# Optimization experiments

Measured on AMD Instinct MI355X. Metric: run time of the kernel, lower is better.

The kernel has to match this reference:

```python
import jax, jax.numpy as jnp
import numpy as np

B, DIM, D_IN, HID, N_HID_EXTRA = 65536, 128, 64, 512, 2  # num_hidden_layers=3 -> 2 extra hidden linears
LOG_SCALE_CLAMP = 2.0


def _mlp(x, Win, bin_, Whid, bhid, Wout, bout):
    # torch nn.Linear: y = x @ W.T + b
    h = jax.nn.relu(x @ Win.T + bin_)
    for i in range(Whid.shape[0]):  # fixed small layer loop
        h = jax.nn.relu(h @ Whid[i].T + bhid[i])
    return h @ Wout.T + bout


def setup_inputs() -> dict:
    key = jax.random.key(0)
    ks = jax.random.split(key, 13)
    w = lambda k, shp: (jax.random.normal(k, shp, dtype=jnp.float32) * 0.05)
    d_out = DIM - D_IN
    return {
        "z": jax.random.normal(ks[0], (B, DIM), dtype=jnp.float32),
        "s_Win": w(ks[1], (HID, D_IN)),   "s_bin": jnp.zeros((HID,), jnp.float32),
        "s_Whid": w(ks[2], (N_HID_EXTRA, HID, HID)), "s_bhid": jnp.zeros((N_HID_EXTRA, HID), jnp.float32),
        "s_Wout": w(ks[3], (d_out, HID)), "s_bout": jnp.zeros((d_out,), jnp.float32),
        "t_Win": w(ks[4], (HID, D_IN)),   "t_bin": jnp.zeros((HID,), jnp.float32),
        "t_Whid": w(ks[5], (N_HID_EXTRA, HID, HID)), "t_bhid": jnp.zeros((N_HID_EXTRA, HID), jnp.float32),
        "t_Wout": w(ks[6], (d_out, HID)), "t_bout": jnp.zeros((d_out,), jnp.float32),
    }


def reference(z, s_Win, s_bin, s_Whid, s_bhid, s_Wout, s_bout,
              t_Win, t_bin, t_Whid, t_bhid, t_Wout, t_bout):
    # mask = first D_IN dims -> gather reduces to slicing
    z1 = z[:, :D_IN]   # (B, d_in)  passthrough half
    z2 = z[:, D_IN:]   # (B, d_out) transformed half
    log_s = jnp.clip(_mlp(z1, s_Win, s_bin, s_Whid, s_bhid, s_Wout, s_bout),
                     -LOG_SCALE_CLAMP, LOG_SCALE_CLAMP)
    t = _mlp(z1, t_Win, t_bin, t_Whid, t_bhid, t_Wout, t_bout)
    z2_out = z2 * jnp.exp(log_s) + t
    z_out = jnp.concatenate([z1, z2_out], axis=1)  # scatter back per mask
    log_det = log_s.sum(axis=-1)                   # (B,)
    return (z_out, log_det)
```

## Files before the change

### kernel.cpp

```cpp
#include <hip/hip_runtime.h>
#include <stdint.h>


#define NROWS 65536
#define RPB   128
#define NBLK  (NROWS / RPB)

#define OFF_S_WIN   0
#define OFF_S_WHID  32768
#define OFF_S_WOUT  557056
#define OFF_T_WIN   589824
#define OFF_T_WHID  622592
#define OFF_T_WOUT  1146880
#define W_ELEMS     1179648

typedef __attribute__((ext_vector_type(8))) short short8;
typedef __attribute__((ext_vector_type(4))) float f32x4;

__device__ __forceinline__ uint32_t f2bf1(float f) {
  uint32_t u = __float_as_uint(f);
  return (u + 0x7fffu + ((u >> 16) & 1u)) >> 16;
}
__device__ __forceinline__ uint32_t pk2bf(float a, float b) {
  return f2bf1(a) | (f2bf1(b) << 16);
}

__global__ void cvt_weights(const float* __restrict__ sWin, const float* __restrict__ sWhid,
                            const float* __restrict__ sWout, const float* __restrict__ tWin,
                            const float* __restrict__ tWhid, const float* __restrict__ tWout,
                            uint16_t* __restrict__ wbf) {
  int g = blockIdx.x * blockDim.x + threadIdx.x;
  int e = g * 4;
  if (e >= W_ELEMS) return;
  const float* src; int off;
  if      (e < OFF_S_WHID) { src = sWin;  off = e; }
  else if (e < OFF_S_WOUT) { src = sWhid; off = e - OFF_S_WHID; }
  else if (e < OFF_T_WIN)  { src = sWout; off = e - OFF_S_WOUT; }
  else if (e < OFF_T_WHID) { src = tWin;  off = e - OFF_T_WIN; }
  else if (e < OFF_T_WOUT) { src = tWhid; off = e - OFF_T_WHID; }
  else                     { src = tWout; off = e - OFF_T_WOUT; }
  f32x4 v = *(const f32x4*)(src + off);
  uint2 r; r.x = pk2bf(v.x, v.y); r.y = pk2bf(v.z, v.w);
  *(uint2*)(wbf + e) = r;
}

template<bool BF>
__device__ __forceinline__ short8 ldW(const uint16_t* __restrict__ wb,
                                      const float* __restrict__ wf, int idx) {
  if (BF) {
    return *(const short8*)(wb + idx);
  } else {
    f32x4 x = *(const f32x4*)(wf + idx);
    f32x4 y = *(const f32x4*)(wf + idx + 4);
    short8 r;
    r[0] = (short)f2bf1(x.x); r[1] = (short)f2bf1(x.y);
    r[2] = (short)f2bf1(x.z); r[3] = (short)f2bf1(x.w);
    r[4] = (short)f2bf1(y.x); r[5] = (short)f2bf1(y.y);
    r[6] = (short)f2bf1(y.z); r[7] = (short)f2bf1(y.w);
    return r;
  }
}

__device__ __forceinline__ short8 ldsB(const uint16_t* buf, int row, int k) {
  int byte = (row * 1024 + k * 2) ^ ((row & 7) << 4);
  return *(const short8*)((const char*)buf + byte);
}

__device__ __forceinline__ void store_h(f32x4 acc[4][8], const float* __restrict__ bias,
                                        uint16_t* hdst, int wave, int lane) {
  const int l15 = lane & 15, lq = lane >> 4;
  __syncthreads();
  #pragma unroll
  for (int rt = 0; rt < 4; ++rt) {
    const int n0 = wave * 64 + rt * 16 + lq * 4;
    f32x4 bv = *(const f32x4*)(bias + n0);
    #pragma unroll
    for (int ct = 0; ct < 8; ++ct) {
      const int row = ct * 16 + l15;
      f32x4 v = acc[rt][ct] + bv;
      uint2 p;
      p.x = pk2bf(fmaxf(v.x, 0.f), fmaxf(v.y, 0.f));
      p.y = pk2bf(fmaxf(v.z, 0.f), fmaxf(v.w, 0.f));
      int byte = (row * 1024 + n0 * 2) ^ ((row & 7) << 4);
      *(uint2*)((char*)hdst + byte) = p;
    }
  }
  __syncthreads();
}

template<bool BF>
__device__ __forceinline__ void dense_in(
    const uint16_t* __restrict__ wb, const float* __restrict__ wf,
    const float* __restrict__ bias, const float* __restrict__ z, long rowbase,
    uint16_t* hdst, int wave, int lane) {
  const int l15 = lane & 15, lq = lane >> 4;
  f32x4 acc[4][8];
  #pragma unroll
  for (int rt = 0; rt < 4; ++rt)
    #pragma unroll
    for (int ct = 0; ct < 8; ++ct) acc[rt][ct] = (f32x4){0.f, 0.f, 0.f, 0.f};
  const int wbase = (wave * 64 + l15) * 64 + lq * 8;
  #pragma unroll
  for (int k0 = 0; k0 < 64; k0 += 32) {
    short8 a[4];
    #pragma unroll
    for (int rt = 0; rt < 4; ++rt) a[rt] = ldW<BF>(wb, wf, wbase + rt * 1024 + k0);
    #pragma unroll
    for (int ct = 0; ct < 8; ++ct) {
      const float* zp = z + (rowbase + ct * 16 + l15) * 128 + lq * 8 + k0;
      f32x4 u = *(const f32x4*)zp;
      f32x4 v = *(const f32x4*)(zp + 4);
      short8 b;
      b[0] = (short)f2bf1(u.x); b[1] = (short)f2bf1(u.y);
      b[2] = (short)f2bf1(u.z); b[3] = (short)f2bf1(u.w);
      b[4] = (short)f2bf1(v.x); b[5] = (short)f2bf1(v.y);
      b[6] = (short)f2bf1(v.z); b[7] = (short)f2bf1(v.w);
      #pragma unroll
      for (int rt = 0; rt < 4; ++rt)
        acc[rt][ct] = __builtin_amdgcn_mfma_f32_16x16x32_bf16(a[rt], b, acc[rt][ct], 0, 0, 0);
    }
  }
  store_h(acc, bias, hdst, wave, lane);
}

template<bool BF>
__device__ __forceinline__ void dense_relu512(
    const uint16_t* __restrict__ wb, const float* __restrict__ wf,
    const float* __restrict__ bias, uint16_t* hbuf, int wave, int lane) {
  const int l15 = lane & 15, lq = lane >> 4;
  f32x4 acc[4][8];
  #pragma unroll
  for (int rt = 0; rt < 4; ++rt)
    #pragma unroll
    for (int ct = 0; ct < 8; ++ct) acc[rt][ct] = (f32x4){0.f, 0.f, 0.f, 0.f};
  const int wbase = (wave * 64 + l15) * 512 + lq * 8;

  short8 an[4];
  #pragma unroll
  for (int rt = 0; rt < 4; ++rt) an[rt] = ldW<BF>(wb, wf, wbase + rt * 8192);

  #pragma unroll 2
  for (int k0 = 0; k0 < 512; k0 += 32) {
    short8 ac[4];
    #pragma unroll
    for (int rt = 0; rt < 4; ++rt) ac[rt] = an[rt];
    if (k0 + 32 < 512) {
      #pragma unroll
      for (int rt = 0; rt < 4; ++rt)
        an[rt] = ldW<BF>(wb, wf, wbase + rt * 8192 + k0 + 32);
    }
    #pragma unroll
    for (int ct = 0; ct < 8; ++ct) {
      short8 b = ldsB(hbuf, ct * 16 + l15, lq * 8 + k0);
      #pragma unroll
      for (int rt = 0; rt < 4; ++rt)
        acc[rt][ct] = __builtin_amdgcn_mfma_f32_16x16x32_bf16(ac[rt], b, acc[rt][ct], 0, 0, 0);
    }
  }
  store_h(acc, bias, hbuf, wave, lane);
}

template<bool BF>
__device__ __forceinline__ void final_layer(
    const uint16_t* __restrict__ wb, const float* __restrict__ wf,
    const uint16_t* hbuf, int wave, int lane, f32x4 acc[4][2]) {
  const int l15 = lane & 15, lq = lane >> 4;
  #pragma unroll
  for (int rt = 0; rt < 4; ++rt)
    #pragma unroll
    for (int ct = 0; ct < 2; ++ct) acc[rt][ct] = (f32x4){0.f, 0.f, 0.f, 0.f};
  const int wbase = l15 * 512 + lq * 8;
  #pragma unroll 4
  for (int k0 = 0; k0 < 512; k0 += 32) {
    short8 a[4];
    #pragma unroll
    for (int rt = 0; rt < 4; ++rt) a[rt] = ldW<BF>(wb, wf, wbase + rt * 8192 + k0);
    #pragma unroll
    for (int ct = 0; ct < 2; ++ct) {
      short8 b = ldsB(hbuf, wave * 32 + ct * 16 + l15, lq * 8 + k0);
      #pragma unroll
      for (int rt = 0; rt < 4; ++rt)
        acc[rt][ct] = __builtin_amdgcn_mfma_f32_16x16x32_bf16(a[rt], b, acc[rt][ct], 0, 0, 0);
    }
  }
}

template<bool BF>
__global__ __launch_bounds__(512, 2) void coupling(
    const float* __restrict__ z,
    const float* __restrict__ sWin, const float* __restrict__ sbin,
    const float* __restrict__ sWhid, const float* __restrict__ sbhid,
    const float* __restrict__ sWout, const float* __restrict__ sbout,
    const float* __restrict__ tWin, const float* __restrict__ tbin,
    const float* __restrict__ tWhid, const float* __restrict__ tbhid,
    const float* __restrict__ tWout, const float* __restrict__ tbout,
    const uint16_t* __restrict__ wbf, float* __restrict__ out) {
  extern __shared__ __align__(16) uint16_t h[];
  const int tid = threadIdx.x;
  const int wave = tid >> 6, lane = tid & 63;
  const int l15 = lane & 15, lq = lane >> 4;
  const long rowbase = (long)blockIdx.x * RPB;

  dense_in<BF>(wbf + OFF_S_WIN, sWin, sbin, z, rowbase, h, wave, lane);
  dense_relu512<BF>(wbf + OFF_S_WHID, sWhid, sbhid, h, wave, lane);
  dense_relu512<BF>(wbf + OFF_S_WHID + 262144, sWhid + 262144, sbhid + 512, h, wave, lane);

  if (wave < 4) {
    f32x4 acc[4][2];
    final_layer<BF>(wbf + OFF_S_WOUT, sWout, h, wave, lane, acc);
    #pragma unroll
    for (int ct = 0; ct < 2; ++ct) {
      const long row = rowbase + wave * 32 + ct * 16 + l15;
      float sum = 0.f;
      #pragma unroll
      for (int rt = 0; rt < 4; ++rt) {
        f32x4 bv = *(const f32x4*)(sbout + rt * 16 + lq * 4);
        f32x4 v = acc[rt][ct] + bv;
        v.x = fminf(fmaxf(v.x, -2.f), 2.f);
        v.y = fminf(fmaxf(v.y, -2.f), 2.f);
        v.z = fminf(fmaxf(v.z, -2.f), 2.f);
        v.w = fminf(fmaxf(v.w, -2.f), 2.f);
        sum += v.x + v.y + v.z + v.w;
        *(f32x4*)(out + row * 128 + 64 + rt * 16 + lq * 4) = v;
      }
      sum += __shfl_xor(sum, 16, 64);
      sum += __shfl_xor(sum, 32, 64);
      if (lane < 16) out[(long)NROWS * 128 + row] = sum;
    }
  } else {
    #pragma unroll
    for (int i = 0; i < 8; ++i) {
      int v = (wave - 4) * 64 + lane + i * 256;
      int row = v >> 4, kc = (v & 15) * 4;
      *(f32x4*)(out + (rowbase + row) * 128 + kc) =
          *(const f32x4*)(z + (rowbase + row) * 128 + kc);
    }
  }
  __syncthreads();

  dense_in<BF>(wbf + OFF_T_WIN, tWin, tbin, z, rowbase, h, wave, lane);
  dense_relu512<BF>(wbf + OFF_T_WHID, tWhid, tbhid, h, wave, lane);
  dense_relu512<BF>(wbf + OFF_T_WHID + 262144, tWhid + 262144, tbhid + 512, h, wave, lane);

  if (wave < 4) {
    f32x4 acc[4][2];
    final_layer<BF>(wbf + OFF_T_WOUT, tWout, h, wave, lane, acc);
    #pragma unroll
    for (int ct = 0; ct < 2; ++ct) {
      const long row = rowbase + wave * 32 + ct * 16 + l15;
      #pragma unroll
      for (int rt = 0; rt < 4; ++rt) {
        f32x4 bv = *(const f32x4*)(tbout + rt * 16 + lq * 4);
        f32x4 tv = acc[rt][ct] + bv;
        const long o = row * 128 + 64 + rt * 16 + lq * 4;
        f32x4 ls = *(const f32x4*)(out + o);
        f32x4 z2 = *(const f32x4*)(z + o);
        f32x4 r;
        r.x = z2.x * __expf(ls.x) + tv.x;
        r.y = z2.y * __expf(ls.y) + tv.y;
        r.z = z2.z * __expf(ls.z) + tv.z;
        r.w = z2.w * __expf(ls.w) + tv.w;
        *(f32x4*)(out + o) = r;
      }
    }
  }
}

extern "C" void kernel_launch(void* const* d_in, const int* in_sizes, int n_in,
                              void* d_out, int out_size, void* d_ws, size_t ws_size,
                              hipStream_t stream) {
  const float* z     = (const float*)d_in[0];
  const float* sWin  = (const float*)d_in[1];
  const float* sbin  = (const float*)d_in[2];
  const float* sWhid = (const float*)d_in[3];
  const float* sbhid = (const float*)d_in[4];
  const float* sWout = (const float*)d_in[5];
  const float* sbout = (const float*)d_in[6];
  const float* tWin  = (const float*)d_in[7];
  const float* tbin  = (const float*)d_in[8];
  const float* tWhid = (const float*)d_in[9];
  const float* tbhid = (const float*)d_in[10];
  const float* tWout = (const float*)d_in[11];
  const float* tbout = (const float*)d_in[12];
  float* out = (float*)d_out;
  const size_t lds_bytes = (size_t)RPB * 512 * sizeof(uint16_t);

  if (ws_size >= (size_t)W_ELEMS * sizeof(uint16_t)) {
    uint16_t* wbf = (uint16_t*)d_ws;
    cvt_weights<<<W_ELEMS / 4 / 256, 256, 0, stream>>>(sWin, sWhid, sWout, tWin, tWhid, tWout, wbf);
    coupling<true><<<NBLK, 512, lds_bytes, stream>>>(z, sWin, sbin, sWhid, sbhid, sWout, sbout,
                                                     tWin, tbin, tWhid, tbhid, tWout, tbout, wbf, out);
  } else {
    coupling<false><<<NBLK, 512, lds_bytes, stream>>>(z, sWin, sbin, sWhid, sbhid, sWout, sbout,
                                                      tWin, tbin, tWhid, tbhid, tWout, tbout,
                                                      (const uint16_t*)d_in[1], out);
  }
}
```

Before: 234.8 us.

## Pad LDS row stride and double-buffer operands in hidden-layer MFMA loop

Replaces the XOR-swizzled LDS layout for the hidden activations with a padded row stride of 1040 bytes, so accesses avoid bank conflicts without the swizzle arithmetic. The 512x512 hidden-layer loop becomes an explicitly double-buffered pipeline: both weight and LDS activation fragments for the next k-slice are prefetched into registers while the current slice's MFMAs run. s_setprio raises wave priority around the MFMA bursts. The cost is more registers held per wave, and the LDS allocation grows slightly.

```diff
diff --git a/kernel.cpp b/kernel.cpp
--- a/kernel.cpp
+++ b/kernel.cpp
@@ -5,6 +5,7 @@
 #define NROWS 65536
 #define RPB   128
 #define NBLK  (NROWS / RPB)
+#define HSTR  1040
 
 #define OFF_S_WIN   0
 #define OFF_S_WHID  32768
@@ -62,8 +63,7 @@
 }
 
 __device__ __forceinline__ short8 ldsB(const uint16_t* buf, int row, int k) {
-  int byte = (row * 1024 + k * 2) ^ ((row & 7) << 4);
-  return *(const short8*)((const char*)buf + byte);
+  return *(const short8*)((const char*)buf + row * HSTR + k * 2);
 }
 
 __device__ __forceinline__ void store_h(f32x4 acc[4][8], const float* __restrict__ bias,
@@ -81,8 +81,7 @@
       uint2 p;
       p.x = pk2bf(fmaxf(v.x, 0.f), fmaxf(v.y, 0.f));
       p.y = pk2bf(fmaxf(v.z, 0.f), fmaxf(v.w, 0.f));
-      int byte = (row * 1024 + n0 * 2) ^ ((row & 7) << 4);
-      *(uint2*)((char*)hdst + byte) = p;
+      *(uint2*)((char*)hdst + row * HSTR + n0 * 2) = p;
     }
   }
   __syncthreads();
@@ -134,28 +133,42 @@
     #pragma unroll
     for (int ct = 0; ct < 8; ++ct) acc[rt][ct] = (f32x4){0.f, 0.f, 0.f, 0.f};
   const int wbase = (wave * 64 + l15) * 512 + lq * 8;
-
-  short8 an[4];
-  #pragma unroll
-  for (int rt = 0; rt < 4; ++rt) an[rt] = ldW<BF>(wb, wf, wbase + rt * 8192);
-
-  #pragma unroll 2
-  for (int k0 = 0; k0 < 512; k0 += 32) {
-    short8 ac[4];
-    #pragma unroll
-    for (int rt = 0; rt < 4; ++rt) ac[rt] = an[rt];
-    if (k0 + 32 < 512) {
+  const char* bbase = (const char*)hbuf + l15 * HSTR + lq * 16;
+
+  short8 a0[4], a1[4], b0[8], b1[8];
+  #pragma unroll
+  for (int rt = 0; rt < 4; ++rt) a0[rt] = ldW<BF>(wb, wf, wbase + rt * 8192);
+  #pragma unroll
+  for (int ct = 0; ct < 8; ++ct) b0[ct] = *(const short8*)(bbase + ct * 16 * HSTR);
+
+  #pragma unroll 1
+  for (int k0 = 0; k0 < 512; k0 += 64) {
+    #pragma unroll
+    for (int rt = 0; rt < 4; ++rt) a1[rt] = ldW<BF>(wb, wf, wbase + rt * 8192 + k0 + 32);
+    #pragma unroll
+    for (int ct = 0; ct < 8; ++ct)
+      b1[ct] = *(const short8*)(bbase + ct * 16 * HSTR + (k0 + 32) * 2);
+    __builtin_amdgcn_s_setprio(1);
+    #pragma unroll
+    for (int ct = 0; ct < 8; ++ct)
       #pragma unroll
       for (int rt = 0; rt < 4; ++rt)
-        an[rt] = ldW<BF>(wb, wf, wbase + rt * 8192 + k0 + 32);
-    }
-    #pragma unroll
-    for (int ct = 0; ct < 8; ++ct) {
-      short8 b = ldsB(hbuf, ct * 16 + l15, lq * 8 + k0);
+        acc[rt][ct] = __builtin_amdgcn_mfma_f32_16x16x32_bf16(a0[rt], b0[ct], acc[rt][ct], 0, 0, 0);
+    __builtin_amdgcn_s_setprio(0);
+    if (k0 < 448) {
+      #pragma unroll
+      for (int rt = 0; rt < 4; ++rt) a0[rt] = ldW<BF>(wb, wf, wbase + rt * 8192 + k0 + 64);
+      #pragma unroll
+      for (int ct = 0; ct < 8; ++ct)
+        b0[ct] = *(const short8*)(bbase + ct * 16 * HSTR + (k0 + 64) * 2);
+    }
+    __builtin_amdgcn_s_setprio(1);
+    #pragma unroll
+    for (int ct = 0; ct < 8; ++ct)
       #pragma unroll
       for (int rt = 0; rt < 4; ++rt)
-        acc[rt][ct] = __builtin_amdgcn_mfma_f32_16x16x32_bf16(ac[rt], b, acc[rt][ct], 0, 0, 0);
-    }
+        acc[rt][ct] = __builtin_amdgcn_mfma_f32_16x16x32_bf16(a1[rt], b1[ct], acc[rt][ct], 0, 0, 0);
+    __builtin_amdgcn_s_setprio(0);
   }
   store_h(acc, bias, hbuf, wave, lane);
 }
@@ -283,7 +296,7 @@
   const float* tWout = (const float*)d_in[11];
   const float* tbout = (const float*)d_in[12];
   float* out = (float*)d_out;
-  const size_t lds_bytes = (size_t)RPB * 512 * sizeof(uint16_t);
+  const size_t lds_bytes = (size_t)RPB * HSTR;
 
   if (ws_size >= (size_t)W_ELEMS * sizeof(uint16_t)) {
     uint16_t* wbf = (uint16_t*)d_ws;
```

Result: slower. 251.8 us (+7.2%).

## Store hidden activations in MFMA-fragment-tiled LDS layout and software-pipeline B loads

Applied to the files above, without the earlier changes.

Hidden activations in LDS move from a row-major XOR-swizzled layout to a tiled layout that matches the MFMA B-fragment order. Each lane can then read its fragment at a fixed stride with no per-access swizzle arithmetic. The 512x512 hidden layer now double-buffers both the weight A-fragments and the LDS B-fragments one step ahead, and raises wave priority around the MFMA bursts. LDS allocation grows by 8 KB so the final prefetch can overrun harmlessly. The aim is to cut LDS address math and load latency stalls in the main GEMM loop, at the cost of slightly more LDS and registers.

```diff
diff --git a/kernel.cpp b/kernel.cpp
--- a/kernel.cpp
+++ b/kernel.cpp
@@ -61,28 +61,22 @@
   }
 }
 
-__device__ __forceinline__ short8 ldsB(const uint16_t* buf, int row, int k) {
-  int byte = (row * 1024 + k * 2) ^ ((row & 7) << 4);
-  return *(const short8*)((const char*)buf + byte);
-}
-
 __device__ __forceinline__ void store_h(f32x4 acc[4][8], const float* __restrict__ bias,
                                         uint16_t* hdst, int wave, int lane) {
   const int l15 = lane & 15, lq = lane >> 4;
   __syncthreads();
+  char* wp = (char*)hdst + wave * 16384 + (lq >> 1) * 2048 + (lq & 1) * 8 + l15 * 16;
   #pragma unroll
   for (int rt = 0; rt < 4; ++rt) {
     const int n0 = wave * 64 + rt * 16 + lq * 4;
     f32x4 bv = *(const f32x4*)(bias + n0);
     #pragma unroll
     for (int ct = 0; ct < 8; ++ct) {
-      const int row = ct * 16 + l15;
       f32x4 v = acc[rt][ct] + bv;
       uint2 p;
       p.x = pk2bf(fmaxf(v.x, 0.f), fmaxf(v.y, 0.f));
       p.y = pk2bf(fmaxf(v.z, 0.f), fmaxf(v.w, 0.f));
-      int byte = (row * 1024 + n0 * 2) ^ ((row & 7) << 4);
-      *(uint2*)((char*)hdst + byte) = p;
+      *(uint2*)(wp + rt * 4096 + ct * 256) = p;
     }
   }
   __syncthreads();
@@ -134,28 +128,35 @@
     #pragma unroll
     for (int ct = 0; ct < 8; ++ct) acc[rt][ct] = (f32x4){0.f, 0.f, 0.f, 0.f};
   const int wbase = (wave * 64 + l15) * 512 + lq * 8;
-
-  short8 an[4];
-  #pragma unroll
-  for (int rt = 0; rt < 4; ++rt) an[rt] = ldW<BF>(wb, wf, wbase + rt * 8192);
-
-  #pragma unroll 2
-  for (int k0 = 0; k0 < 512; k0 += 32) {
-    short8 ac[4];
-    #pragma unroll
-    for (int rt = 0; rt < 4; ++rt) ac[rt] = an[rt];
-    if (k0 + 32 < 512) {
+  const char* bb = (const char*)hbuf + l15 * 16 + lq * 2048;
+
+  short8 a[2][4];
+  #pragma unroll
+  for (int rt = 0; rt < 4; ++rt) a[0][rt] = ldW<BF>(wb, wf, wbase + rt * 8192);
+  short8 bcur = *(const short8*)bb;
+
+  #pragma unroll 1
+  for (int ko = 0; ko < 512; ko += 128) {
+    #pragma unroll
+    for (int kk = 0; kk < 4; ++kk) {
+      int kn = ko + kk * 32 + 32;
+      if (kn > 480) kn = 480;
       #pragma unroll
       for (int rt = 0; rt < 4; ++rt)
-        an[rt] = ldW<BF>(wb, wf, wbase + rt * 8192 + k0 + 32);
-    }
-    #pragma unroll
-    for (int ct = 0; ct < 8; ++ct) {
-      short8 b = ldsB(hbuf, ct * 16 + l15, lq * 8 + k0);
-      #pragma unroll
-      for (int rt = 0; rt < 4; ++rt)
-        acc[rt][ct] = __builtin_amdgcn_mfma_f32_16x16x32_bf16(ac[rt], b, acc[rt][ct], 0, 0, 0);
-    }
+        a[(kk + 1) & 1][rt] = ldW<BF>(wb, wf, wbase + rt * 8192 + kn);
+      __builtin_amdgcn_s_setprio(1);
+      #pragma unroll
+      for (int ct = 0; ct < 8; ++ct) {
+        const int noff = (ct < 7) ? (kk * 8192 + (ct + 1) * 256) : ((kk + 1) * 8192);
+        short8 bn = *(const short8*)(bb + noff);
+        #pragma unroll
+        for (int rt = 0; rt < 4; ++rt)
+          acc[rt][ct] = __builtin_amdgcn_mfma_f32_16x16x32_bf16(a[kk & 1][rt], bcur, acc[rt][ct], 0, 0, 0);
+        bcur = bn;
+      }
+      __builtin_amdgcn_s_setprio(0);
+    }
+    bb += 32768;
   }
   store_h(acc, bias, hbuf, wave, lane);
 }
@@ -170,18 +171,24 @@
     #pragma unroll
     for (int ct = 0; ct < 2; ++ct) acc[rt][ct] = (f32x4){0.f, 0.f, 0.f, 0.f};
   const int wbase = l15 * 512 + lq * 8;
-  #pragma unroll 4
-  for (int k0 = 0; k0 < 512; k0 += 32) {
-    short8 a[4];
-    #pragma unroll
-    for (int rt = 0; rt < 4; ++rt) a[rt] = ldW<BF>(wb, wf, wbase + rt * 8192 + k0);
-    #pragma unroll
-    for (int ct = 0; ct < 2; ++ct) {
-      short8 b = ldsB(hbuf, wave * 32 + ct * 16 + l15, lq * 8 + k0);
+  const char* fb = (const char*)hbuf + (wave * 32 + l15) * 16 + lq * 2048;
+  #pragma unroll 1
+  for (int ko = 0; ko < 512; ko += 128) {
+    #pragma unroll
+    for (int kk = 0; kk < 4; ++kk) {
+      short8 a[4];
       #pragma unroll
       for (int rt = 0; rt < 4; ++rt)
-        acc[rt][ct] = __builtin_amdgcn_mfma_f32_16x16x32_bf16(a[rt], b, acc[rt][ct], 0, 0, 0);
-    }
+        a[rt] = ldW<BF>(wb, wf, wbase + rt * 8192 + ko + kk * 32);
+      #pragma unroll
+      for (int ct = 0; ct < 2; ++ct) {
+        short8 b = *(const short8*)(fb + kk * 8192 + ct * 256);
+        #pragma unroll
+        for (int rt = 0; rt < 4; ++rt)
+          acc[rt][ct] = __builtin_amdgcn_mfma_f32_16x16x32_bf16(a[rt], b, acc[rt][ct], 0, 0, 0);
+      }
+    }
+    fb += 32768;
   }
 }
 
@@ -283,7 +290,7 @@
   const float* tWout = (const float*)d_in[11];
   const float* tbout = (const float*)d_in[12];
   float* out = (float*)d_out;
-  const size_t lds_bytes = (size_t)RPB * 512 * sizeof(uint16_t);
+  const size_t lds_bytes = 139264;
 
   if (ws_size >= (size_t)W_ELEMS * sizeof(uint16_t)) {
     uint16_t* wbf = (uint16_t*)d_ws;
```

New measurement: 238.5 us. About the same (+1.6%).
